# Kernel optimization log

Hardware: AMD Instinct MI355X
Metric: run time of the kernel (lower is better)

The kernel has to match this reference:

```python
import jax, jax.numpy as jnp
import numpy as np

B, C, T = 8, 256, 2048
K = 10                     # n_neigh_seq
TEMPORAL_SCALE = 2048
SHORT_RATIO = 0.4
STITCH_GAP = 20


def setup_inputs() -> dict:
    key = jax.random.key(0)
    k1, k2, k3, k4 = jax.random.split(key, 4)
    x = jax.random.normal(k1, (B, C, T), dtype=jnp.float32)
    num_frms = jax.random.randint(k2, (B,), 0, 2048, dtype=jnp.int64 if jax.config.jax_enable_x64 else jnp.int32)
    W_conv = jax.random.normal(k3, (C, C, 3), dtype=jnp.float32) * 0.02  # Conv1d(out,in,k)
    b_conv = jnp.zeros((C,), dtype=jnp.float32)
    W_mlp = jax.random.normal(k4, (C, 2 * C), dtype=jnp.float32) * 0.02  # Linear(2C -> C)
    b_mlp = jnp.zeros((C,), dtype=jnp.float32)
    return {"x": x, "num_frms": num_frms, "W_conv": W_conv, "b_conv": b_conv,
            "W_mlp": W_mlp, "b_mlp": b_mlp}


def knn_neigh_idx(x, num_frms, k=K):
    """Vectorized translation of knn() + get_neigh_idx_semantic()."""
    b, c, t = x.shape
    ratio = TEMPORAL_SCALE / t
    half1 = k // 2
    half2 = k - half1
    # pairwise squared distances via ||xi||^2 + ||xj||^2 - 2 xi.xj (same math,
    # avoids the B*C*T*T intermediate the torch code materializes)
    sq = jnp.sum(x * x, axis=1)                           # [B,T]
    gram = jnp.einsum('bci,bcj->bij', x, x)               # [B,T,T]
    dif = sq[:, :, None] + sq[:, None, :] - 2.0 * gram    # [B,T,T]
    _, idx_org = jax.lax.top_k(-dif, k)                   # smallest-k -> [B,T,k]
    big = jnp.max(dif) + 1.0
    # per-batch short-video rewiring (original does a python loop over batch)
    cond = num_frms.astype(jnp.float32) <= SHORT_RATIO * TEMPORAL_SCALE   # [B]
    thr = (num_frms.astype(jnp.float32) + STITCH_GAP) / ratio             # [B]
    pos = jnp.arange(t)
    region = (pos[None, :, None] >= thr[:, None, None]) & \
             (pos[None, None, :] >= thr[:, None, None])                   # [B,T,T]
    dif_m = jnp.where(region, big, dif)
    # kill the already-chosen first half of neighbors, then re-topk the rest
    b_idx = jnp.arange(b)[:, None, None]
    r_idx = pos[None, :, None]
    dif_m = dif_m.at[b_idx, r_idx, idx_org[:, :, :half1]].set(big)
    _, idx2 = jax.lax.top_k(-dif_m, half2)                # [B,T,half2]
    tail = jnp.where(cond[:, None, None], idx2, idx_org[:, :, half1:])
    idx_new = jnp.concatenate([idx_org[:, :, :half1], tail], axis=-1)     # [B,T,k]
    shift = (jnp.arange(b) * t)[:, None, None]
    return (idx_new + shift).reshape(-1)                  # [B*T*k] flat node ids


def reference(x, num_frms, W_conv, b_conv, W_mlp, b_mlp):
    b, c, t = x.shape
    # tconv1: Conv1d k=3, s=1, p=1
    c_out = jax.lax.conv_general_dilated(
        x, W_conv, window_strides=(1,), padding=[(1, 1)],
        dimension_numbers=('NCH', 'OIH', 'NCH')) + b_conv[None, :, None]   # [B,C,T]
    # NeighConv on raw x (gcn_insert == 'par'), nfeat_mode='feat_ctr', agg='max'
    neigh = knn_neigh_idx(x, num_frms)                    # [B*T*K]
    feat = jnp.transpose(x, (0, 2, 1)).reshape(-1, c)     # [B*T, C]
    feat_neigh = feat[neigh].reshape(-1, K, c)            # [B*T, K, C]
    ctr = jnp.broadcast_to(feat[:, None, :], feat_neigh.shape)
    cat = jnp.concatenate([feat_neigh, ctr], axis=-1)     # [B*T, K, 2C]
    g = jnp.einsum('nkd,od->nko', cat, W_mlp) + b_mlp     # [B*T, K, C]
    g = jnp.max(g, axis=1)                                # max aggregation
    g_out = jnp.transpose(g.reshape(b, t, -1), (0, 2, 1)) # [B,C,T]
    out = jax.nn.relu(c_out + g_out)
    # MaxPool1d(kernel=2, stride=2)
    out = out.reshape(b, out.shape[1], t // 2, 2).max(axis=-1)
    return out
```

## Files before the change

kernel.cpp:

```cpp
#include <hip/hip_runtime.h>
#include <hip/hip_bf16.h>
#include <math.h>
#include <float.h>

#define NC 256
#define NT 2048

typedef __attribute__((ext_vector_type(4))) float f32x4;
typedef __attribute__((ext_vector_type(8))) short short8;
typedef __attribute__((ext_vector_type(8))) unsigned short ushort8;

#define SQ_OFF 0
#define A_OFF  131072
#define XL_OFF 8388608
#define E_OFF  16908288
#define NB_OFF 33685504

__device__ __forceinline__ int load_nf(const int* __restrict__ nf, int b) {
    bool is64 = (nf[1] == 0) & (nf[3] == 0) & (nf[5] == 0) & (nf[7] == 0);
    return is64 ? nf[2 * b] : nf[b];
}

__device__ __forceinline__ void split_bf16(float f, unsigned short& h, unsigned short& l) {
    __hip_bfloat16 hb = __float2bfloat16(f);
    float fh = __bfloat162float(hb);
    __hip_bfloat16 lb = __float2bfloat16(f - fh);
    h = *(unsigned short*)&hb;
    l = *(unsigned short*)&lb;
}

__device__ __forceinline__ float rl_f(float v, int srclane) {
    return __int_as_float(__builtin_amdgcn_readlane(__float_as_int(v), srclane));
}
__device__ __forceinline__ int rl_i(int v, int srclane) {
    return __builtin_amdgcn_readlane(v, srclane);
}
__device__ __forceinline__ float dpp_shr1_f(float v) {
    return __int_as_float(__builtin_amdgcn_update_dpp(0, __float_as_int(v), 0x111, 0xf, 0xf, false));
}
__device__ __forceinline__ int dpp_shr1_i(int v) {
    return __builtin_amdgcn_update_dpp(0, v, 0x111, 0xf, 0xf, false);
}

__global__ __launch_bounds__(256) void k_sqt(const float* __restrict__ x, double* __restrict__ sq,
                                             unsigned short* __restrict__ Xh8,
                                             unsigned short* __restrict__ Xl8,
                                             float* __restrict__ xT) {
    __shared__ double part[32][33];
    int b = blockIdx.y;
    int q0 = blockIdx.x * 32;
    int tid = threadIdx.x;
    int tq = tid & 7;
    int cg = tid >> 3;
    const float* xp = x + (size_t)b * NC * NT + q0 + tq * 4;
    double a0 = 0.0, a1 = 0.0, a2 = 0.0, a3 = 0.0;
    ushort8 hv[4], lw[4];
    float xv[4][8];
    #pragma unroll
    for (int i = 0; i < 8; ++i) {
        int c = cg * 8 + i;
        float4 f4 = *(const float4*)&xp[(size_t)c * NT];
        unsigned short h, l;
        split_bf16(f4.x, h, l); hv[0][i] = h; lw[0][i] = l; xv[0][i] = f4.x;
        a0 = fma((double)f4.x, (double)f4.x, a0);
        split_bf16(f4.y, h, l); hv[1][i] = h; lw[1][i] = l; xv[1][i] = f4.y;
        a1 = fma((double)f4.y, (double)f4.y, a1);
        split_bf16(f4.z, h, l); hv[2][i] = h; lw[2][i] = l; xv[2][i] = f4.z;
        a2 = fma((double)f4.z, (double)f4.z, a2);
        split_bf16(f4.w, h, l); hv[3][i] = h; lw[3][i] = l; xv[3][i] = f4.w;
        a3 = fma((double)f4.w, (double)f4.w, a3);
    }
    #pragma unroll
    for (int j = 0; j < 4; ++j) {
        int t = q0 + tq * 4 + j;
        size_t off = (((size_t)b * 32 + cg) * NT + t) * 8;
        *(ushort8*)(Xh8 + off) = hv[j];
        *(ushort8*)(Xl8 + off) = lw[j];
        float* xtr = &xT[((size_t)b * NT + t) * NC + cg * 8];
        *(float4*)xtr       = *(float4*)&xv[j][0];
        *(float4*)(xtr + 4) = *(float4*)&xv[j][4];
    }
    part[tq * 4 + 0][cg] = a0;
    part[tq * 4 + 1][cg] = a1;
    part[tq * 4 + 2][cg] = a2;
    part[tq * 4 + 3][cg] = a3;
    __syncthreads();
    if (tid < 32) {
        double s = 0.0;
        #pragma unroll
        for (int g = 0; g < 32; ++g) s += part[tid][g];
        sq[b * NT + q0 + tid] = s;
    }
}

__global__ __launch_bounds__(256) void k_wsplit(const float* __restrict__ Wc, const float* __restrict__ Wm,
                                                unsigned short* __restrict__ wsc) {
    int o = blockIdx.x;
    int tid = threadIdx.x;
    #pragma unroll
    for (int i = 0; i < 3; ++i) {
        int idx = i * 256 + tid;
        int c = idx / 3, kh = idx % 3;
        float w = Wc[(size_t)o * 768 + idx];
        if (kh == 1) w += Wm[(size_t)o * 512 + 256 + c];
        unsigned short h, l;
        split_bf16(w, h, l);
        wsc[(size_t)(kh * 256 + o) * 256 + c] = h;
        wsc[196608 + (size_t)(kh * 256 + o) * 256 + c] = l;
    }
    float wa = Wm[(size_t)o * 512 + tid];
    unsigned short h, l;
    split_bf16(wa, h, l);
    wsc[393216 + (size_t)o * 256 + tid] = h;
    wsc[458752 + (size_t)o * 256 + tid] = l;
}

#define XQH_S 264
#define DFB_S 130

#define LD_CHUNK(chx, ph, pl) do { \
    size_t o_ = ((size_t)(((chx) & 7) * 4 + quad) * NT + (size_t)((((chx) >> 3) << 7) + n0)) * 8; \
    ph = *(const short8*)(Xh8b + o_); \
    pl = *(const short8*)(Xl8b + o_); \
  } while (0)

__global__ __launch_bounds__(512, 8) void k_knn_a(const unsigned short* __restrict__ Xh8,
                                                  const unsigned short* __restrict__ Xl8,
                                                  const double* __restrict__ sq,
                                                  const int* __restrict__ nf,
                                                  unsigned short* __restrict__ cand,
                                                  unsigned short* __restrict__ cand2) {
    __shared__ __align__(16) unsigned short Qh[16 * XQH_S];
    __shared__ __align__(16) unsigned short Ql[16 * XQH_S];
    __shared__ __align__(16) float Df[2][16 * DFB_S];
    int t_wg = blockIdx.x;
    int u = t_wg >> 7;
    int q0 = ((t_wg >> 3) & 127) * 16;
    int b = (t_wg + u) & 7;
    int tid = threadIdx.x;
    int lane = tid & 63, wave = tid >> 6;
    const unsigned short* Xh8b = Xh8 + (size_t)b * 32 * NT * 8;
    const unsigned short* Xl8b = Xl8 + (size_t)b * 32 * NT * 8;
    const double* sqb = sq + b * NT;
    int n = load_nf(nf, b);
    int thr = n + 20;
    bool need2 = (n <= 819) && (q0 + 15 >= thr);
    float lv[2], lv2[2];
    int li[2], li2[2];
    #pragma unroll
    for (int rr = 0; rr < 2; ++rr) { lv[rr] = INFINITY; li[rr] = 0; lv2[rr] = INFINITY; li2[rr] = 0; }
    {
        int q = tid & 15, cgp = tid >> 4;
        size_t off = (((size_t)cgp) * NT + q0 + q) * 8;
        uint4 vh = *(const uint4*)(Xh8b + off);
        uint4 vl = *(const uint4*)(Xl8b + off);
        *(uint4*)&Qh[q * XQH_S + cgp * 8] = vh;
        *(uint4*)&Ql[q * XQH_S + cgp * 8] = vl;
    }
    int quad = lane >> 4, l15 = lane & 15;
    int qrow = l15;
    int n0 = wave * 16 + l15;
    float sqv[4];
    #pragma unroll
    for (int bb = 0; bb < 4; ++bb) sqv[bb] = (float)sqb[q0 + quad * 4 + bb];
    __syncthreads();
    const int nch = (NT / 128) * 8;
    short8 hA[2], lA[2];
    LD_CHUNK(0, hA[0], lA[0]);
    LD_CHUNK(1, hA[1], lA[1]);
    int ch = 0;
    for (int k0 = 0; k0 < NT; k0 += 128) {
        f32x4 acc0 = {0.f, 0.f, 0.f, 0.f};
        float sk0 = (float)sqb[k0 + n0];
        #pragma unroll
        for (int cc = 0; cc < 8; ++cc) {
            const int bi = cc & 1;
            short8 bh = hA[bi], bl = lA[bi];
            int chn = ch + 2;
            if (chn > nch - 1) chn = nch - 1;
            LD_CHUNK(chn, hA[bi], lA[bi]);
            int cb = cc << 5;
            short8 ah = *(const short8*)&Qh[qrow * XQH_S + cb + quad * 8];
            short8 al = *(const short8*)&Ql[qrow * XQH_S + cb + quad * 8];
            acc0 = __builtin_amdgcn_mfma_f32_16x16x32_bf16(al, bh, acc0, 0, 0, 0);
            acc0 = __builtin_amdgcn_mfma_f32_16x16x32_bf16(ah, bl, acc0, 0, 0, 0);
            acc0 = __builtin_amdgcn_mfma_f32_16x16x32_bf16(ah, bh, acc0, 0, 0, 0);
            ++ch;
        }
        int p = (k0 >> 7) & 1;
        float* DfP = Df[p];
        #pragma unroll
        for (int bb = 0; bb < 4; ++bb) {
            int mr = quad * 4 + bb;
            DfP[mr * DFB_S + n0] = sqv[bb] + sk0 - 2.f * acc0[bb];
        }
        __syncthreads();
        #pragma unroll
        for (int rr = 0; rr < 2; ++rr) {
            int row = wave * 2 + rr;
            #pragma unroll
            for (int g = 0; g < 2; ++g) {
                float d = DfP[row * DFB_S + g * 64 + lane];
                int kbase = k0 + g * 64;
                {
                    float thr16 = rl_f(lv[rr], 15);
                    unsigned long long mask = __ballot(d < thr16);
                    while (mask) {
                        int bit = __ffsll(mask) - 1;
                        mask &= mask - 1;
                        float vv = rl_f(d, bit);
                        int jj = kbase + bit;
                        unsigned long long le = __ballot(lv[rr] <= vv);
                        int pos = __popcll(le);
                        float pv = dpp_shr1_f(lv[rr]);
                        int pj = dpp_shr1_i(li[rr]);
                        if (lane < 16) {
                            if (lane == pos)      { lv[rr] = vv; li[rr] = jj; }
                            else if (lane > pos)  { lv[rr] = pv; li[rr] = pj; }
                        }
                        mask &= __ballot(d < rl_f(lv[rr], 15));
                    }
                }
                bool do2 = need2 && (kbase < thr);
                if (do2) {
                    unsigned long long vmask = __ballot((kbase + lane) < thr);
                    float thr24 = rl_f(lv2[rr], 23);
                    unsigned long long mask = __ballot(d < thr24) & vmask;
                    while (mask) {
                        int bit = __ffsll(mask) - 1;
                        mask &= mask - 1;
                        float vv = rl_f(d, bit);
                        int jj = kbase + bit;
                        unsigned long long le = __ballot(lv2[rr] <= vv);
                        int pos = __popcll(le);
                        float pv = dpp_shr1_f(lv2[rr]);
                        int pj = dpp_shr1_i(li2[rr]);
                        if (lane == 16) { pv = rl_f(lv2[rr], 15); pj = rl_i(li2[rr], 15); }
                        if (lane < 24) {
                            if (lane == pos)      { lv2[rr] = vv; li2[rr] = jj; }
                            else if (lane > pos)  { lv2[rr] = pv; li2[rr] = pj; }
                        }
                        mask &= __ballot(d < rl_f(lv2[rr], 23));
                    }
                }
            }
        }
    }
    if (lane < 16) {
        #pragma unroll
        for (int rr = 0; rr < 2; ++rr)
            cand[((size_t)b * NT + q0 + wave * 2 + rr) * 16 + lane] = (unsigned short)li[rr];
    }
    if (need2 && lane < 24) {
        #pragma unroll
        for (int rr = 0; rr < 2; ++rr) {
            unsigned short v = (lv2[rr] == INFINITY) ? 0xFFFFu : (unsigned short)li2[rr];
            cand2[((size_t)b * NT + q0 + wave * 2 + rr) * 24 + lane] = v;
        }
    }
}

__global__ __launch_bounds__(256) void k_rr(const float* __restrict__ xT, const double* __restrict__ sq,
                                            const int* __restrict__ nf,
                                            const unsigned short* __restrict__ cand,
                                            const unsigned short* __restrict__ cand2,
                                            int* __restrict__ nb) {
    int b = blockIdx.y;
    int wave = threadIdx.x >> 6, lane = threadIdx.x & 63;
    int t = blockIdx.x * 4 + wave;
    int n = load_nf(nf, b);
    int thr = n + 20;
    bool rr2row = (n <= 819) && (t >= thr);
    const float* qp = &xT[((size_t)b * NT + t) * NC];
    float4 q4 = *(const float4*)&qp[lane * 4];
    double sqt = sq[b * NT + t];
    int* nrow = &nb[((size_t)b * NT + t) * 10];
    const unsigned short* cr = &cand[((size_t)b * NT + t) * 16];
    double myd = 0.0; int myc = 0;
    for (int i = 0; i < 16; ++i) {
        int t2 = cr[i];
        float4 k4 = *(const float4*)&xT[((size_t)b * NT + t2) * NC + lane * 4];
        double s = fma((double)q4.w, (double)k4.w,
                   fma((double)q4.z, (double)k4.z,
                   fma((double)q4.y, (double)k4.y, (double)q4.x * (double)k4.x)));
        #pragma unroll
        for (int off = 32; off; off >>= 1) s += __shfl_xor(s, off);
        double d = sqt + sq[b * NT + t2] - 2.0 * s;
        if (lane == i) { myd = d; myc = t2; }
    }
    int rank = 0;
    for (int j = 0; j < 16; ++j) {
        double dj = __shfl(myd, j);
        int cj = __shfl(myc, j);
        if (lane < 16 && j != lane)
            rank += ((dj < myd) || (dj == myd && cj < myc)) ? 1 : 0;
    }
    if (lane < 16 && rank < 5) nrow[rank] = myc;
    bool w1hi = (lane < 16) && (rank >= 5) && (rank < 10);
    if (!rr2row) {
        if (w1hi) nrow[rank] = myc;
        return;
    }
    int f[5];
    #pragma unroll
    for (int s = 0; s < 5; ++s) {
        unsigned long long m = __ballot((lane < 16) && (rank == s));
        f[s] = __shfl(myc, __ffsll(m) - 1);
    }
    const unsigned short* cr2 = &cand2[((size_t)b * NT + t) * 24];
    double myd2 = DBL_MAX; int myc2 = 0x7FFFFFFF;
    for (int i = 0; i < 24; ++i) {
        int c16 = cr2[i];
        if (c16 == 0xFFFF) continue;
        int t2 = c16;
        float4 k4 = *(const float4*)&xT[((size_t)b * NT + t2) * NC + lane * 4];
        double s = fma((double)q4.w, (double)k4.w,
                   fma((double)q4.z, (double)k4.z,
                   fma((double)q4.y, (double)k4.y, (double)q4.x * (double)k4.x)));
        #pragma unroll
        for (int off = 32; off; off >>= 1) s += __shfl_xor(s, off);
        double d = sqt + sq[b * NT + t2] - 2.0 * s;
        if (lane == i) { myd2 = d; myc2 = t2; }
    }
    bool keep = (lane < 24) && (myc2 != 0x7FFFFFFF);
    #pragma unroll
    for (int s = 0; s < 5; ++s) keep = keep && (myc2 != f[s]);
    int rank2 = 0;
    for (int j = 0; j < 24; ++j) {
        double dj = __shfl(myd2, j);
        int cj = __shfl(myc2, j);
        bool kj = __shfl((int)keep, j);
        if (keep && kj && j != lane)
            rank2 += ((dj < myd2) || (dj == myd2 && cj < myc2)) ? 1 : 0;
    }
    int nK = __popcll(__ballot(keep)); if (nK > 5) nK = 5;
    if (keep && rank2 < 5) nrow[5 + rank2] = myc2;
    if (w1hi && (rank - 5) >= nK) nrow[rank] = myc;
}

#define XT_S 40

__global__ __launch_bounds__(256) void k_conv(const float* __restrict__ x, const unsigned short* __restrict__ wsc,
                                              const float* __restrict__ bc, const float* __restrict__ bm,
                                              float* __restrict__ E, float* __restrict__ A) {
    __shared__ __align__(16) unsigned short XTh[66 * XT_S], XTl[66 * XT_S];
    __shared__ __align__(16) unsigned short Wsh[3 * 64 * XT_S], Wsl[3 * 64 * XT_S];
    __shared__ __align__(16) unsigned short Wah[64 * XT_S], Wal[64 * XT_S];
    int tx = blockIdx.x * 64, oy = blockIdx.y * 64, b = blockIdx.z;
    int tid = threadIdx.x, lane = tid & 63, wave = tid >> 6;
    int quad = lane >> 4, l15 = lane & 15;
    f32x4 accE[4] = {}, accA[4] = {};
    for (int c0 = 0; c0 < 256; c0 += 32) {
        __syncthreads();
        #pragma unroll
        for (int i = 0; i < 8; ++i) {
            int c = wave * 8 + i;
            int t = lane;
            int g = tx - 1 + t;
            float v = (g >= 0 && g < NT) ? x[((size_t)b * NC + c0 + c) * NT + g] : 0.f;
            unsigned short h, l;
            split_bf16(v, h, l);
            XTh[t * XT_S + c] = h;
            XTl[t * XT_S + c] = l;
        }
        if (tid < 64) {
            int c = tid >> 1, t = 64 + (tid & 1);
            int g = tx - 1 + t;
            float v = (g < NT) ? x[((size_t)b * NC + c0 + c) * NT + g] : 0.f;
            unsigned short h, l;
            split_bf16(v, h, l);
            XTh[t * XT_S + c] = h;
            XTl[t * XT_S + c] = l;
        }
        #pragma unroll
        for (int i = 0; i < 3; ++i) {
            int gidx = i * 256 + tid;
            int kh = gidx >> 8;
            int o  = (gidx >> 2) & 63;
            int g4 = gidx & 3;
            uint4 vh = *(const uint4*)&wsc[(size_t)(kh * 256 + oy + o) * 256 + c0 + g4 * 8];
            *(uint4*)&Wsh[(kh * 64 + o) * XT_S + g4 * 8] = vh;
            uint4 vl = *(const uint4*)&wsc[196608 + (size_t)(kh * 256 + oy + o) * 256 + c0 + g4 * 8];
            *(uint4*)&Wsl[(kh * 64 + o) * XT_S + g4 * 8] = vl;
        }
        {
            int o = tid >> 2, g4 = tid & 3;
            uint4 vh = *(const uint4*)&wsc[393216 + (size_t)(oy + o) * 256 + c0 + g4 * 8];
            *(uint4*)&Wah[o * XT_S + g4 * 8] = vh;
            uint4 vl = *(const uint4*)&wsc[458752 + (size_t)(oy + o) * 256 + c0 + g4 * 8];
            *(uint4*)&Wal[o * XT_S + g4 * 8] = vl;
        }
        __syncthreads();
        int trow = wave * 16 + l15;
        short8 a_h[3], a_l[3];
        #pragma unroll
        for (int kh = 0; kh < 3; ++kh) {
            a_h[kh] = *(const short8*)&XTh[(trow + kh) * XT_S + quad * 8];
            a_l[kh] = *(const short8*)&XTl[(trow + kh) * XT_S + quad * 8];
        }
        #pragma unroll
        for (int ns = 0; ns < 4; ++ns) {
            int orow = ns * 16 + l15;
            short8 wa_h = *(const short8*)&Wah[orow * XT_S + quad * 8];
            short8 wa_l = *(const short8*)&Wal[orow * XT_S + quad * 8];
            accA[ns] = __builtin_amdgcn_mfma_f32_16x16x32_bf16(a_l[1], wa_h, accA[ns], 0, 0, 0);
            accA[ns] = __builtin_amdgcn_mfma_f32_16x16x32_bf16(a_h[1], wa_l, accA[ns], 0, 0, 0);
            accA[ns] = __builtin_amdgcn_mfma_f32_16x16x32_bf16(a_h[1], wa_h, accA[ns], 0, 0, 0);
            #pragma unroll
            for (int kh = 0; kh < 3; ++kh) {
                short8 w_h = *(const short8*)&Wsh[(kh * 64 + orow) * XT_S + quad * 8];
                short8 w_l = *(const short8*)&Wsl[(kh * 64 + orow) * XT_S + quad * 8];
                accE[ns] = __builtin_amdgcn_mfma_f32_16x16x32_bf16(a_l[kh], w_h, accE[ns], 0, 0, 0);
                accE[ns] = __builtin_amdgcn_mfma_f32_16x16x32_bf16(a_h[kh], w_l, accE[ns], 0, 0, 0);
                accE[ns] = __builtin_amdgcn_mfma_f32_16x16x32_bf16(a_h[kh], w_h, accE[ns], 0, 0, 0);
            }
        }
    }
    #pragma unroll
    for (int ns = 0; ns < 4; ++ns) {
        int o = oy + ns * 16 + l15;
        float bias = bc[o] + bm[o];
        #pragma unroll
        for (int r = 0; r < 4; ++r) {
            int t = tx + wave * 16 + quad * 4 + r;
            E[((size_t)b * NT + t) * 256 + o] = accE[ns][r] + bias;
            A[((size_t)b * NT + t) * 256 + o] = accA[ns][r];
        }
    }
}

__global__ __launch_bounds__(256) void k_epi(const float* __restrict__ A, const float* __restrict__ E,
                                             const int* __restrict__ nb, float* __restrict__ out) {
    __shared__ float buf[8 * 260];
    int p0 = blockIdx.x * 8;
    int b = blockIdx.y;
    int tid = threadIdx.x;
    int o4 = tid & 63;
    int pg = tid >> 6;
    #pragma unroll
    for (int pp2 = 0; pp2 < 2; ++pp2) {
        int pp = pg * 2 + pp2;
        int p = p0 + pp;
        float vm[4] = {0.f, 0.f, 0.f, 0.f};
        #pragma unroll
        for (int tt = 0; tt < 2; ++tt) {
            int t = p * 2 + tt;
            const int* nrow = &nb[((size_t)b * NT + t) * 10];
            float gm[4] = {-FLT_MAX, -FLT_MAX, -FLT_MAX, -FLT_MAX};
            #pragma unroll
            for (int k = 0; k < 10; ++k) {
                int t2 = nrow[k] & (NT - 1);
                float4 a = *(const float4*)&A[((size_t)b * NT + t2) * 256 + o4 * 4];
                gm[0] = fmaxf(gm[0], a.x); gm[1] = fmaxf(gm[1], a.y);
                gm[2] = fmaxf(gm[2], a.z); gm[3] = fmaxf(gm[3], a.w);
            }
            float4 e = *(const float4*)&E[((size_t)b * NT + t) * 256 + o4 * 4];
            vm[0] = fmaxf(vm[0], fmaxf(e.x + gm[0], 0.f));
            vm[1] = fmaxf(vm[1], fmaxf(e.y + gm[1], 0.f));
            vm[2] = fmaxf(vm[2], fmaxf(e.z + gm[2], 0.f));
            vm[3] = fmaxf(vm[3], fmaxf(e.w + gm[3], 0.f));
        }
        float4 v = {vm[0], vm[1], vm[2], vm[3]};
        *(float4*)&buf[pp * 260 + o4 * 4] = v;
    }
    __syncthreads();
    #pragma unroll
    for (int i = 0; i < 8; ++i) {
        int idx = tid + i * 256;
        int oo = idx >> 3, pp = idx & 7;
        out[((size_t)b * 256 + oo) * 1024 + p0 + pp] = buf[pp * 260 + oo];
    }
}

extern "C" void kernel_launch(void* const* d_in, const int* in_sizes, int n_in,
                              void* d_out, int out_size, void* d_ws, size_t ws_size,
                              hipStream_t stream) {
    const float* x  = (const float*)d_in[0];
    const int*   nf = (const int*)d_in[1];
    const float* Wc = (const float*)d_in[2];
    const float* bc = (const float*)d_in[3];
    const float* Wm = (const float*)d_in[4];
    const float* bm = (const float*)d_in[5];
    float* out = (float*)d_out;
    char* ws = (char*)d_ws;
    double* sq = (double*)(ws + SQ_OFF);
    float* A   = (float*)(ws + A_OFF);
    float* E   = (float*)(ws + E_OFF);
    int* nb    = (int*)(ws + NB_OFF);
    unsigned short* Xh8 = (unsigned short*)(ws + A_OFF);
    unsigned short* Xl8 = (unsigned short*)(ws + A_OFF + XL_OFF);
    float* xT = (float*)(ws + E_OFF);
    unsigned short* wsc   = (unsigned short*)d_out;
    unsigned short* cand  = (unsigned short*)d_out + (1 << 20);
    unsigned short* cand2 = (unsigned short*)d_out + (1 << 20) + (1 << 19);

    k_sqt<<<dim3(64, 8), dim3(256), 0, stream>>>(x, sq, Xh8, Xl8, xT);
    k_wsplit<<<dim3(256), dim3(256), 0, stream>>>(Wc, Wm, wsc);
    k_knn_a<<<dim3(1024), dim3(512), 0, stream>>>(Xh8, Xl8, sq, nf, cand, cand2);
    k_rr<<<dim3(512, 8), dim3(256), 0, stream>>>(xT, sq, nf, cand, cand2, nb);
    k_conv<<<dim3(32, 4, 8), dim3(256), 0, stream>>>(x, wsc, bc, bm, E, A);
    k_epi<<<dim3(128, 8), dim3(256), 0, stream>>>(A, E, nb, out);
}
```

Baseline: 424.8 us.

## Fuse KNN candidate re-ranking into the KNN search kernel

The double-precision re-rank of the 16/24 candidates now runs inside k_knn_a, reading candidate indices straight from registers via lane reads. This drops the separate k_rr launch and the cand/cand2 round trip through global memory. The grid mapping also changes from a swizzled 1D layout that interleaved batches to a plain (128,8) grid. The cost is that the serial re-rank tail now runs inside a large-LDS 512-thread kernel, which may lengthen that kernel and lose the batch-interleaving benefit.

Result: faster. 401.1 us (median of 2 runs) (-5.6%).

```diff
diff --git a/kernel.cpp b/kernel.cpp
--- a/kernel.cpp
+++ b/kernel.cpp
@@ -128,15 +128,13 @@
                                                   const unsigned short* __restrict__ Xl8,
                                                   const double* __restrict__ sq,
                                                   const int* __restrict__ nf,
-                                                  unsigned short* __restrict__ cand,
-                                                  unsigned short* __restrict__ cand2) {
+                                                  const float* __restrict__ xT,
+                                                  int* __restrict__ nb) {
     __shared__ __align__(16) unsigned short Qh[16 * XQH_S];
     __shared__ __align__(16) unsigned short Ql[16 * XQH_S];
     __shared__ __align__(16) float Df[2][16 * DFB_S];
-    int t_wg = blockIdx.x;
-    int u = t_wg >> 7;
-    int q0 = ((t_wg >> 3) & 127) * 16;
-    int b = (t_wg + u) & 7;
+    int q0 = blockIdx.x * 16;
+    int b = blockIdx.y;
     int tid = threadIdx.x;
     int lane = tid & 63, wave = tid >> 6;
     const unsigned short* Xh8b = Xh8 + (size_t)b * 32 * NT * 8;
@@ -246,96 +244,74 @@
             }
         }
     }
-    if (lane < 16) {
-        #pragma unroll
-        for (int rr = 0; rr < 2; ++rr)
-            cand[((size_t)b * NT + q0 + wave * 2 + rr) * 16 + lane] = (unsigned short)li[rr];
-    }
-    if (need2 && lane < 24) {
-        #pragma unroll
-        for (int rr = 0; rr < 2; ++rr) {
-            unsigned short v = (lv2[rr] == INFINITY) ? 0xFFFFu : (unsigned short)li2[rr];
-            cand2[((size_t)b * NT + q0 + wave * 2 + rr) * 24 + lane] = v;
-        }
-    }
-}
-
-__global__ __launch_bounds__(256) void k_rr(const float* __restrict__ xT, const double* __restrict__ sq,
-                                            const int* __restrict__ nf,
-                                            const unsigned short* __restrict__ cand,
-                                            const unsigned short* __restrict__ cand2,
-                                            int* __restrict__ nb) {
-    int b = blockIdx.y;
-    int wave = threadIdx.x >> 6, lane = threadIdx.x & 63;
-    int t = blockIdx.x * 4 + wave;
-    int n = load_nf(nf, b);
-    int thr = n + 20;
-    bool rr2row = (n <= 819) && (t >= thr);
-    const float* qp = &xT[((size_t)b * NT + t) * NC];
-    float4 q4 = *(const float4*)&qp[lane * 4];
-    double sqt = sq[b * NT + t];
-    int* nrow = &nb[((size_t)b * NT + t) * 10];
-    const unsigned short* cr = &cand[((size_t)b * NT + t) * 16];
-    double myd = 0.0; int myc = 0;
-    for (int i = 0; i < 16; ++i) {
-        int t2 = cr[i];
-        float4 k4 = *(const float4*)&xT[((size_t)b * NT + t2) * NC + lane * 4];
-        double s = fma((double)q4.w, (double)k4.w,
-                   fma((double)q4.z, (double)k4.z,
-                   fma((double)q4.y, (double)k4.y, (double)q4.x * (double)k4.x)));
-        #pragma unroll
-        for (int off = 32; off; off >>= 1) s += __shfl_xor(s, off);
-        double d = sqt + sq[b * NT + t2] - 2.0 * s;
-        if (lane == i) { myd = d; myc = t2; }
-    }
-    int rank = 0;
-    for (int j = 0; j < 16; ++j) {
-        double dj = __shfl(myd, j);
-        int cj = __shfl(myc, j);
-        if (lane < 16 && j != lane)
-            rank += ((dj < myd) || (dj == myd && cj < myc)) ? 1 : 0;
-    }
-    if (lane < 16 && rank < 5) nrow[rank] = myc;
-    bool w1hi = (lane < 16) && (rank >= 5) && (rank < 10);
-    if (!rr2row) {
-        if (w1hi) nrow[rank] = myc;
-        return;
-    }
-    int f[5];
-    #pragma unroll
-    for (int s = 0; s < 5; ++s) {
-        unsigned long long m = __ballot((lane < 16) && (rank == s));
-        f[s] = __shfl(myc, __ffsll(m) - 1);
-    }
-    const unsigned short* cr2 = &cand2[((size_t)b * NT + t) * 24];
-    double myd2 = DBL_MAX; int myc2 = 0x7FFFFFFF;
-    for (int i = 0; i < 24; ++i) {
-        int c16 = cr2[i];
-        if (c16 == 0xFFFF) continue;
-        int t2 = c16;
-        float4 k4 = *(const float4*)&xT[((size_t)b * NT + t2) * NC + lane * 4];
-        double s = fma((double)q4.w, (double)k4.w,
-                   fma((double)q4.z, (double)k4.z,
-                   fma((double)q4.y, (double)k4.y, (double)q4.x * (double)k4.x)));
-        #pragma unroll
-        for (int off = 32; off; off >>= 1) s += __shfl_xor(s, off);
-        double d = sqt + sq[b * NT + t2] - 2.0 * s;
-        if (lane == i) { myd2 = d; myc2 = t2; }
-    }
-    bool keep = (lane < 24) && (myc2 != 0x7FFFFFFF);
-    #pragma unroll
-    for (int s = 0; s < 5; ++s) keep = keep && (myc2 != f[s]);
-    int rank2 = 0;
-    for (int j = 0; j < 24; ++j) {
-        double dj = __shfl(myd2, j);
-        int cj = __shfl(myc2, j);
-        bool kj = __shfl((int)keep, j);
-        if (keep && kj && j != lane)
-            rank2 += ((dj < myd2) || (dj == myd2 && cj < myc2)) ? 1 : 0;
-    }
-    int nK = __popcll(__ballot(keep)); if (nK > 5) nK = 5;
-    if (keep && rank2 < 5) nrow[5 + rank2] = myc2;
-    if (w1hi && (rank - 5) >= nK) nrow[rank] = myc;
+#undef LD_CHUNK
+    const float* xTb = xT + (size_t)b * NT * NC;
+    for (int rr = 0; rr < 2; ++rr) {
+        int t = q0 + wave * 2 + rr;
+        bool rr2row = (n <= 819) && (t >= thr);
+        float4 q4 = *(const float4*)&xTb[(size_t)t * NC + lane * 4];
+        double sqt = sqb[t];
+        int* nrow = &nb[((size_t)b * NT + t) * 10];
+        double myd = 0.0; int myc = 0;
+        for (int i = 0; i < 16; ++i) {
+            int t2 = rl_i(li[rr], i);
+            float4 k4 = *(const float4*)&xTb[(size_t)t2 * NC + lane * 4];
+            double s = fma((double)q4.w, (double)k4.w,
+                       fma((double)q4.z, (double)k4.z,
+                       fma((double)q4.y, (double)k4.y, (double)q4.x * (double)k4.x)));
+            #pragma unroll
+            for (int off = 32; off; off >>= 1) s += __shfl_xor(s, off);
+            double d = sqt + sqb[t2] - 2.0 * s;
+            if (lane == i) { myd = d; myc = t2; }
+        }
+        int rank = 0;
+        for (int j = 0; j < 16; ++j) {
+            double dj = __shfl(myd, j);
+            int cj = __shfl(myc, j);
+            if (lane < 16 && j != lane)
+                rank += ((dj < myd) || (dj == myd && cj < myc)) ? 1 : 0;
+        }
+        if (lane < 16 && rank < 5) nrow[rank] = myc;
+        bool w1hi = (lane < 16) && (rank >= 5) && (rank < 10);
+        if (!rr2row) {
+            if (w1hi) nrow[rank] = myc;
+            continue;
+        }
+        int f[5];
+        #pragma unroll
+        for (int s = 0; s < 5; ++s) {
+            unsigned long long m = __ballot((lane < 16) && (rank == s));
+            f[s] = __shfl(myc, __ffsll(m) - 1);
+        }
+        double myd2 = DBL_MAX; int myc2 = 0x7FFFFFFF;
+        for (int i = 0; i < 24; ++i) {
+            float v2 = rl_f(lv2[rr], i);
+            if (v2 == INFINITY) continue;
+            int t2 = rl_i(li2[rr], i);
+            float4 k4 = *(const float4*)&xTb[(size_t)t2 * NC + lane * 4];
+            double s = fma((double)q4.w, (double)k4.w,
+                       fma((double)q4.z, (double)k4.z,
+                       fma((double)q4.y, (double)k4.y, (double)q4.x * (double)k4.x)));
+            #pragma unroll
+            for (int off = 32; off; off >>= 1) s += __shfl_xor(s, off);
+            double d = sqt + sqb[t2] - 2.0 * s;
+            if (lane == i) { myd2 = d; myc2 = t2; }
+        }
+        bool keep = (lane < 24) && (myc2 != 0x7FFFFFFF);
+        #pragma unroll
+        for (int s = 0; s < 5; ++s) keep = keep && (myc2 != f[s]);
+        int rank2 = 0;
+        for (int j = 0; j < 24; ++j) {
+            double dj = __shfl(myd2, j);
+            int cj = __shfl(myc2, j);
+            bool kj = __shfl((int)keep, j);
+            if (keep && kj && j != lane)
+                rank2 += ((dj < myd2) || (dj == myd2 && cj < myc2)) ? 1 : 0;
+        }
+        int nK = __popcll(__ballot(keep)); if (nK > 5) nK = 5;
+        if (keep && rank2 < 5) nrow[5 + rank2] = myc2;
+        if (w1hi && (rank - 5) >= nK) nrow[rank] = myc;
+    }
 }
 
 #define XT_S 40
@@ -490,14 +466,11 @@
     unsigned short* Xh8 = (unsigned short*)(ws + A_OFF);
     unsigned short* Xl8 = (unsigned short*)(ws + A_OFF + XL_OFF);
     float* xT = (float*)(ws + E_OFF);
-    unsigned short* wsc   = (unsigned short*)d_out;
-    unsigned short* cand  = (unsigned short*)d_out + (1 << 20);
-    unsigned short* cand2 = (unsigned short*)d_out + (1 << 20) + (1 << 19);
+    unsigned short* wsc = (unsigned short*)d_out;
 
     k_sqt<<<dim3(64, 8), dim3(256), 0, stream>>>(x, sq, Xh8, Xl8, xT);
     k_wsplit<<<dim3(256), dim3(256), 0, stream>>>(Wc, Wm, wsc);
-    k_knn_a<<<dim3(1024), dim3(512), 0, stream>>>(Xh8, Xl8, sq, nf, cand, cand2);
-    k_rr<<<dim3(512, 8), dim3(256), 0, stream>>>(xT, sq, nf, cand, cand2, nb);
+    k_knn_a<<<dim3(128, 8), dim3(512), 0, stream>>>(Xh8, Xl8, sq, nf, xT, nb);
     k_conv<<<dim3(32, 4, 8), dim3(256), 0, stream>>>(x, wsc, bc, bm, E, A);
     k_epi<<<dim3(128, 8), dim3(256), 0, stream>>>(A, E, nb, out);
 }
```
